# Kernel optimization log

Measured on AMD Instinct MI355X. Metric: run time of the kernel, lower is better.

## Reference

```python
import jax, jax.numpy as jnp
import numpy as np

N_NODES = 100000
N_EDGES = 1600000
IN_CH, HID_CH, OUT_CH = 128, 128, 40


def setup_inputs() -> dict:
    key = jax.random.key(0)
    ks = jax.random.split(key, 7)
    s = 1.0 / np.sqrt(IN_CH)
    s2 = 1.0 / np.sqrt(HID_CH)
    return {
        "x": jax.random.normal(ks[0], (N_NODES, IN_CH), jnp.float32),
        "edge_index": jax.random.randint(ks[1], (2, N_EDGES), 0, N_NODES, jnp.int64),
        "W1l": jax.random.normal(ks[2], (IN_CH, HID_CH), jnp.float32) * s,
        "b1": jnp.zeros((HID_CH,), jnp.float32),
        "W1r": jax.random.normal(ks[3], (IN_CH, HID_CH), jnp.float32) * s,
        "W2l": jax.random.normal(ks[4], (HID_CH, OUT_CH), jnp.float32) * s2,
        "b2": jnp.zeros((OUT_CH,), jnp.float32),
        "W2r": jax.random.normal(ks[5], (HID_CH, OUT_CH), jnp.float32) * s2,
    }


def reference(x, edge_index, W1l, b1, W1r, W2l, b2, W2r):
    src, dst = edge_index[0], edge_index[1]
    # per-target in-degree for mean aggregation (zero-degree nodes -> 0 output)
    deg = jax.ops.segment_sum(jnp.ones((src.shape[0],), x.dtype), dst,
                              num_segments=N_NODES)
    inv_deg = jnp.where(deg > 0, 1.0 / jnp.maximum(deg, 1.0), 0.0)[:, None]

    def sage(h, Wl, b, Wr):
        # gather source features, scatter-sum to targets, normalize -> mean
        agg = jax.ops.segment_sum(h[src], dst, num_segments=N_NODES) * inv_deg
        return agg @ Wl + b + h @ Wr

    h = jax.nn.relu(sage(x, W1l, b1, W1r))
    # F.dropout(p=0.5) defaults to training=True -> active dropout
    keep = jax.random.bernoulli(jax.random.key(42), 0.5, h.shape)
    h = jnp.where(keep, h * 2.0, 0.0)
    out = sage(h, W2l, b2, W2r)
    return jax.nn.log_softmax(out, axis=1)
```

## Files before the change

kernel.cpp:

```cpp
#include <hip/hip_runtime.h>
#include <stdint.h>
#include <stddef.h>

#define N_NODES 100000
#define N_EDGES 1600000
#define IN_CH 128
#define HID_CH 128
#define OUT_CH 40

#define NB 196
#define GCAP 10240
#define TILE_EDGES 2048
#define LCAP 40

#define N_MASK_WORDS 400000
#define N_CVT8 1600000

#define WROW 264
#define WROW2 136

#define QSCALE 21.25f
#define QSTEP  0.047058824f

typedef __attribute__((ext_vector_type(8))) short bf16x8;
typedef __attribute__((ext_vector_type(8))) unsigned short u16x8;
typedef __attribute__((ext_vector_type(4))) float f32x4;

__device__ __forceinline__ ushort f2bf(float f) {
    uint32_t u = __float_as_uint(f);
    uint32_t r = (u + 0x7FFFu + ((u >> 16) & 1u)) >> 16;
    return (ushort)r;
}
__device__ __forceinline__ float bf2f(ushort u) {
    return __uint_as_float(((uint32_t)u) << 16);
}

__device__ __forceinline__ uint32_t rotl32(uint32_t x, int r) {
    return (x << r) | (x >> (32 - r));
}

__device__ __forceinline__ void threefry2x32_k42(uint32_t x0, uint32_t x1,
                                                 uint32_t& o0, uint32_t& o1) {
    const uint32_t ks0 = 0u, ks1 = 42u;
    const uint32_t ks2 = 0u ^ 42u ^ 0x1BD11BDAu;
    x0 += ks0; x1 += ks1;
    x0 += x1; x1 = rotl32(x1, 13); x1 ^= x0;
    x0 += x1; x1 = rotl32(x1, 15); x1 ^= x0;
    x0 += x1; x1 = rotl32(x1, 26); x1 ^= x0;
    x0 += x1; x1 = rotl32(x1,  6); x1 ^= x0;
    x0 += ks1; x1 += ks2 + 1u;
    x0 += x1; x1 = rotl32(x1, 17); x1 ^= x0;
    x0 += x1; x1 = rotl32(x1, 29); x1 ^= x0;
    x0 += x1; x1 = rotl32(x1, 16); x1 ^= x0;
    x0 += x1; x1 = rotl32(x1, 24); x1 ^= x0;
    x0 += ks2; x1 += ks0 + 2u;
    x0 += x1; x1 = rotl32(x1, 13); x1 ^= x0;
    x0 += x1; x1 = rotl32(x1, 15); x1 ^= x0;
    x0 += x1; x1 = rotl32(x1, 26); x1 ^= x0;
    x0 += x1; x1 = rotl32(x1,  6); x1 ^= x0;
    x0 += ks0; x1 += ks1 + 3u;
    x0 += x1; x1 = rotl32(x1, 17); x1 ^= x0;
    x0 += x1; x1 = rotl32(x1, 29); x1 ^= x0;
    x0 += x1; x1 = rotl32(x1, 16); x1 ^= x0;
    x0 += x1; x1 = rotl32(x1, 24); x1 ^= x0;
    x0 += ks1; x1 += ks2 + 4u;
    x0 += x1; x1 = rotl32(x1, 13); x1 ^= x0;
    x0 += x1; x1 = rotl32(x1, 15); x1 ^= x0;
    x0 += x1; x1 = rotl32(x1, 26); x1 ^= x0;
    x0 += x1; x1 = rotl32(x1,  6); x1 ^= x0;
    x0 += ks2; x1 += ks0 + 5u;
    o0 = x0; o1 = x1;
}

__device__ __forceinline__ void load_edge(const void* ei, bool is32, int e,
                                          int& s, int& d) {
    if (is32) {
        const int* p = (const int*)ei;
        s = p[e]; d = p[N_EDGES + e];
    } else {
        const long long* p = (const long long*)ei;
        s = (int)p[e]; d = (int)p[N_EDGES + e];
    }
}

__global__ __launch_bounds__(256) void prep(const int* __restrict__ ei32,
                                            int* __restrict__ flag,
                                            int* __restrict__ gcnt) {
    const int t = threadIdx.x;
    if (blockIdx.x == 0) {
        __shared__ int red[256];
        int local = 0;
        #pragma unroll
        for (int j = 0; j < 64; ++j) {
            int k = (t * 64 + j) * 97;
            local |= ei32[2 * k + 1];
        }
        red[t] = local;
        __syncthreads();
        for (int off = 128; off; off >>= 1) {
            if (t < off) red[t] |= red[t + off];
            __syncthreads();
        }
        if (t == 0) *flag = (red[0] != 0);
    } else {
        for (int i = t; i < NB * 16; i += 256) gcnt[i] = 0;
    }
}

__global__ __launch_bounds__(256) void bucket_edges(
    const void* __restrict__ ei, const int* __restrict__ flag,
    int* __restrict__ gcnt, uint2* __restrict__ gbuf) {
    __shared__ uint2 lbuf[NB][LCAP];
    __shared__ int lcnt[NB];
    const bool is32 = (*flag != 0);
    const int t = threadIdx.x;
    for (int b = t; b < NB; b += 256) lcnt[b] = 0;
    __syncthreads();
    const int base = blockIdx.x * TILE_EDGES;
    #pragma unroll
    for (int j = 0; j < TILE_EDGES / 256; ++j) {
        int e = base + j * 256 + t;
        if (e < N_EDGES) {
            int s, d;
            load_edge(ei, is32, e, s, d);
            int b = d >> 9;
            int pos = atomicAdd(&lcnt[b], 1);
            if (pos < LCAP) {
                lbuf[b][pos] = make_uint2((uint32_t)s, (uint32_t)d);
            } else {
                int gp = atomicAdd(&gcnt[b * 16], 1);
                gbuf[(size_t)b * GCAP + gp] = make_uint2((uint32_t)s, (uint32_t)d);
            }
        }
    }
    __syncthreads();
    if (t < NB) {
        int cnt = lcnt[t];
        if (cnt > LCAP) cnt = LCAP;
        if (cnt > 0) {
            int gp = atomicAdd(&gcnt[t * 16], cnt);
            uint2* dst = gbuf + (size_t)t * GCAP + gp;
            for (int i = 0; i < cnt; ++i) dst[i] = lbuf[t][i];
        }
    }
}

__global__ void bucket_scan(const int* __restrict__ gcnt, int* __restrict__ bbase) {
    __shared__ int s[256];
    int t = threadIdx.x;
    int tot = (t < NB) ? gcnt[t * 16] : 0;
    s[t] = tot;
    __syncthreads();
    for (int off = 1; off < 256; off <<= 1) {
        int a = (t >= off) ? s[t - off] : 0;
        __syncthreads();
        s[t] += a;
        __syncthreads();
    }
    if (t < NB) bbase[t] = s[t] - tot;
}

__global__ __launch_bounds__(256) void build_csr(
    const int* __restrict__ gcnt, const uint2* __restrict__ gbuf,
    const int* __restrict__ bbase, int* __restrict__ csr, int* __restrict__ cursor) {
    __shared__ int hist[512];
    __shared__ int excl[512];
    __shared__ int cur[512];
    __shared__ int psum[256];
    const int b = blockIdx.x;
    const int t = threadIdx.x;
    hist[t] = 0; hist[t + 256] = 0;
    __syncthreads();
    const int base = bbase[b];
    const int cnt = gcnt[b * 16];
    const uint2* src = gbuf + (size_t)b * GCAP;
    for (int i = t; i < cnt; i += 256)
        atomicAdd(&hist[src[i].y & 511], 1);
    __syncthreads();
    int h0 = hist[2 * t], h1 = hist[2 * t + 1];
    psum[t] = h0 + h1;
    __syncthreads();
    int v = psum[t];
    for (int off = 1; off < 256; off <<= 1) {
        int a = (t >= off) ? psum[t - off] : 0;
        __syncthreads();
        psum[t] += a;
        __syncthreads();
    }
    int pex = psum[t] - v;
    excl[2 * t] = pex;
    excl[2 * t + 1] = pex + h0;
    cur[2 * t] = pex;
    cur[2 * t + 1] = pex + h0;
    __syncthreads();
    for (int j = t; j < 512; j += 256) {
        int node = b * 512 + j;
        if (node < N_NODES) cursor[node] = base + excl[j] + hist[j];
    }
    for (int i = t; i < cnt; i += 256) {
        uint2 p = src[i];
        int pos = atomicAdd(&cur[p.y & 511], 1);
        csr[base + pos] = (int)p.x;
    }
}

__device__ __forceinline__ uint32_t q4(float a, float b, float c, float d) {
    int qa = (int)rintf(a * QSCALE + 128.0f);
    int qb = (int)rintf(b * QSCALE + 128.0f);
    int qc = (int)rintf(c * QSCALE + 128.0f);
    int qd = (int)rintf(d * QSCALE + 128.0f);
    qa = min(max(qa, 0), 255);
    qb = min(max(qb, 0), 255);
    qc = min(max(qc, 0), 255);
    qd = min(max(qd, 0), 255);
    return (uint32_t)qa | ((uint32_t)qb << 8) | ((uint32_t)qc << 16) | ((uint32_t)qd << 24);
}

__global__ __launch_bounds__(256) void cvt_and_mask(
    const float* __restrict__ in, ushort* __restrict__ out,
    uint32_t* __restrict__ xu8, uint32_t* __restrict__ mask) {
    const long gid = (long)blockIdx.x * blockDim.x + threadIdx.x;
    const long stride = (long)gridDim.x * blockDim.x;
    for (long i = gid; i < N_CVT8; i += stride) {
        float4 v0 = *reinterpret_cast<const float4*>(in + i * 8);
        float4 v1 = *reinterpret_cast<const float4*>(in + i * 8 + 4);
        u16x8 r;
        r[0] = f2bf(v0.x); r[1] = f2bf(v0.y); r[2] = f2bf(v0.z); r[3] = f2bf(v0.w);
        r[4] = f2bf(v1.x); r[5] = f2bf(v1.y); r[6] = f2bf(v1.z); r[7] = f2bf(v1.w);
        *reinterpret_cast<u16x8*>(out + i * 8) = r;
        uint2 p;
        p.x = q4(v0.x, v0.y, v0.z, v0.w);
        p.y = q4(v1.x, v1.y, v1.z, v1.w);
        *reinterpret_cast<uint2*>(xu8 + i * 2) = p;
    }
    for (long w = gid; w < N_MASK_WORDS; w += stride) {
        uint32_t m = 0;
        #pragma unroll 4
        for (int j = 0; j < 32; ++j) {
            uint32_t o0, o1;
            threefry2x32_k42(0u, (uint32_t)w * 32u + j, o0, o1);
            m |= ((o0 ^ o1) >> 31) << j;
        }
        mask[w] = m;
    }
}

__global__ void cvt_w2(const float* __restrict__ W1l, const float* __restrict__ W1r,
                       const float* __restrict__ W2l, const float* __restrict__ W2r,
                       ushort* __restrict__ Wt1, ushort* __restrict__ Wt2) {
    int blk = blockIdx.x;
    int k = threadIdx.x;
    if (blk < 128) {
        int n = blk;
        float v = (k < 128) ? W1l[(size_t)k * 128 + n] : W1r[(size_t)(k - 128) * 128 + n];
        Wt1[(size_t)n * 256 + k] = f2bf(v);
    } else if (k < 128) {
        int n = blk - 128;
        float v = (n < OUT_CH) ? W2l[(size_t)k * 40 + n]
                               : W2r[(size_t)k * 40 + (n - OUT_CH)];
        Wt2[(size_t)n * 128 + k] = f2bf(v);
    }
}

__global__ __launch_bounds__(256) void aggregate_mean_u8(
    const uint32_t* __restrict__ feat8, const int* __restrict__ csr,
    const int* __restrict__ cursor, ushort* __restrict__ out) {
    int node = blockIdx.x * 4 + (threadIdx.x >> 6);
    if (node >= N_NODES) return;
    const int lane = threadIdx.x & 63;
    const int g = lane >> 4;
    const int c = lane & 15;
    const int beg = (node > 0) ? cursor[node - 1] : 0;
    const int end = cursor[node];
    const int deg = end - beg;

    int myidx = (lane < deg) ? csr[beg + lane] : 0;

    float acc[8];
    #pragma unroll
    for (int j = 0; j < 8; ++j) acc[j] = 0.0f;

    const int nfull = (deg < 64) ? deg : 64;
    const int niter = (nfull + 3) >> 2;
    #pragma unroll 4
    for (int k = 0; k < niter; ++k) {
        int e = g + 4 * k;
        bool valid = (e < nfull);
        int es = valid ? e : 0;
        int s = __shfl(myidx, es, 64);
        float w = valid ? 1.0f : 0.0f;
        uint2 v = *reinterpret_cast<const uint2*>(feat8 + (size_t)s * 32 + c * 2);
        acc[0] += w * (float)(v.x & 0xffu);
        acc[1] += w * (float)((v.x >> 8) & 0xffu);
        acc[2] += w * (float)((v.x >> 16) & 0xffu);
        acc[3] += w * (float)(v.x >> 24);
        acc[4] += w * (float)(v.y & 0xffu);
        acc[5] += w * (float)((v.y >> 8) & 0xffu);
        acc[6] += w * (float)((v.y >> 16) & 0xffu);
        acc[7] += w * (float)(v.y >> 24);
    }
    for (int e = 64 + g; e < deg; e += 4) {
        int s = csr[beg + e];
        uint2 v = *reinterpret_cast<const uint2*>(feat8 + (size_t)s * 32 + c * 2);
        acc[0] += (float)(v.x & 0xffu);
        acc[1] += (float)((v.x >> 8) & 0xffu);
        acc[2] += (float)((v.x >> 16) & 0xffu);
        acc[3] += (float)(v.x >> 24);
        acc[4] += (float)(v.y & 0xffu);
        acc[5] += (float)((v.y >> 8) & 0xffu);
        acc[6] += (float)((v.y >> 16) & 0xffu);
        acc[7] += (float)(v.y >> 24);
    }

    #pragma unroll
    for (int j = 0; j < 8; ++j) {
        acc[j] += __shfl_xor(acc[j], 16, 64);
        acc[j] += __shfl_xor(acc[j], 32, 64);
    }

    if (g == 0) {
        float inv = (deg > 0) ? (1.0f / (float)deg) : 0.0f;
        u16x8 r;
        #pragma unroll
        for (int j = 0; j < 8; ++j) {
            float m = (deg > 0) ? (acc[j] * inv - 128.0f) * QSTEP : 0.0f;
            r[j] = f2bf(m);
        }
        *reinterpret_cast<u16x8*>(out + (size_t)node * 128 + c * 8) = r;
    }
}

__global__ __launch_bounds__(256) void layer1_mfma(
    const ushort* __restrict__ agg, const ushort* __restrict__ xbf,
    const ushort* __restrict__ Wt, const float* __restrict__ b1,
    const uint32_t* __restrict__ dmask, ushort* __restrict__ h) {
    __shared__ ushort wlds[64 * WROW];
    const int tid = threadIdx.x;
    const int lane = tid & 63;
    const int l15 = lane & 15, kg = lane >> 4;
    const int colBase = (blockIdx.x & 1) * 64;
    const int row_base = ((blockIdx.x >> 1) * 4 + (tid >> 6)) * 16;

    #pragma unroll
    for (int i = 0; i < 8; ++i) {
        int idx = tid + i * 256;
        int r = idx >> 5, c = idx & 31;
        u16x8 v = *reinterpret_cast<const u16x8*>(Wt + (size_t)(colBase + r) * 256 + c * 8);
        *reinterpret_cast<u16x8*>(wlds + r * WROW + c * 8) = v;
    }
    __syncthreads();
    if (row_base >= N_NODES) return;

    int r0 = row_base + l15;
    int r0c = (r0 < N_NODES) ? r0 : (N_NODES - 1);

    bf16x8 a[8];
    #pragma unroll
    for (int ks = 0; ks < 4; ++ks) {
        a[ks]     = *reinterpret_cast<const bf16x8*>(agg + (size_t)r0c * 128 + ks * 32 + kg * 8);
        a[ks + 4] = *reinterpret_cast<const bf16x8*>(xbf + (size_t)r0c * 128 + ks * 32 + kg * 8);
    }

    f32x4 acc[4];
    #pragma unroll
    for (int nf = 0; nf < 4; ++nf) acc[nf] = (f32x4){0.f, 0.f, 0.f, 0.f};

    #pragma unroll
    for (int nf = 0; nf < 4; ++nf) {
        const ushort* bp = wlds + (nf * 16 + l15) * WROW + kg * 8;
        #pragma unroll
        for (int ks = 0; ks < 8; ++ks) {
            bf16x8 b = *reinterpret_cast<const bf16x8*>(bp + ks * 32);
            acc[nf] = __builtin_amdgcn_mfma_f32_16x16x32_bf16(a[ks], b, acc[nf], 0, 0, 0);
        }
    }

    #pragma unroll
    for (int r = 0; r < 4; ++r) {
        int row = row_base + kg * 4 + r;
        if (row < N_NODES) {
            uint4 mw = *reinterpret_cast<const uint4*>(dmask + (size_t)row * 4);
            const uint32_t* mwp = reinterpret_cast<const uint32_t*>(&mw);
            #pragma unroll
            for (int nf = 0; nf < 4; ++nf) {
                int col = colBase + nf * 16 + l15;
                float v = acc[nf][r] + b1[col];
                v = fmaxf(v, 0.0f) * 2.0f;
                if ((mwp[col >> 5] >> (col & 31)) & 1u) v = 0.0f;
                h[(size_t)row * 128 + col] = f2bf(v);
            }
        }
    }
}

__global__ __launch_bounds__(256) void layer2_pre(
    const ushort* __restrict__ hbf, const ushort* __restrict__ Wt2,
    ushort* __restrict__ y2z2) {
    __shared__ ushort wlds[80 * WROW2];
    const int tid = threadIdx.x;
    const int lane = tid & 63;
    const int l15 = lane & 15, kg = lane >> 4;
    const int row_base = (blockIdx.x * 4 + (tid >> 6)) * 16;

    #pragma unroll
    for (int i = 0; i < 5; ++i) {
        int idx = tid + i * 256;
        int r = idx >> 4, c = idx & 15;
        u16x8 v = *reinterpret_cast<const u16x8*>(Wt2 + (size_t)r * 128 + c * 8);
        *reinterpret_cast<u16x8*>(wlds + r * WROW2 + c * 8) = v;
    }
    __syncthreads();
    if (row_base >= N_NODES) return;

    int r0 = row_base + l15;
    int r0c = (r0 < N_NODES) ? r0 : (N_NODES - 1);

    bf16x8 a[4];
    #pragma unroll
    for (int ks = 0; ks < 4; ++ks)
        a[ks] = *reinterpret_cast<const bf16x8*>(hbf + (size_t)r0c * 128 + ks * 32 + kg * 8);

    f32x4 acc[5];
    #pragma unroll
    for (int nf = 0; nf < 5; ++nf) acc[nf] = (f32x4){0.f, 0.f, 0.f, 0.f};

    #pragma unroll
    for (int nf = 0; nf < 5; ++nf) {
        const ushort* bp = wlds + (nf * 16 + l15) * WROW2 + kg * 8;
        #pragma unroll
        for (int ks = 0; ks < 4; ++ks) {
            bf16x8 b = *reinterpret_cast<const bf16x8*>(bp + ks * 32);
            acc[nf] = __builtin_amdgcn_mfma_f32_16x16x32_bf16(a[ks], b, acc[nf], 0, 0, 0);
        }
    }

    #pragma unroll
    for (int r = 0; r < 4; ++r) {
        int row = row_base + kg * 4 + r;
        if (row < N_NODES) {
            #pragma unroll
            for (int nf = 0; nf < 5; ++nf) {
                int col = nf * 16 + l15;
                y2z2[(size_t)row * 80 + col] = f2bf(acc[nf][r]);
            }
        }
    }
}

__global__ __launch_bounds__(256) void aggregate_mean_40(
    const ushort* __restrict__ y2, const int* __restrict__ csr,
    const int* __restrict__ cursor, ushort* __restrict__ aggy2) {
    int node = blockIdx.x * 4 + (threadIdx.x >> 6);
    if (node >= N_NODES) return;
    const int lane = threadIdx.x & 63;
    const int g = lane >> 3;
    const int c = lane & 7;
    const int cc = (c < 5) ? c : (c - 5);
    const float cw = (c < 5) ? 1.0f : 0.0f;
    const int beg = (node > 0) ? cursor[node - 1] : 0;
    const int end = cursor[node];
    const int deg = end - beg;

    int myidx = (lane < deg) ? csr[beg + lane] : 0;

    float acc[8];
    #pragma unroll
    for (int j = 0; j < 8; ++j) acc[j] = 0.0f;

    const int nfull = (deg < 64) ? deg : 64;
    const int niter = (nfull + 7) >> 3;
    for (int k = 0; k < niter; ++k) {
        int e = g + 8 * k;
        bool valid = (e < nfull);
        int es = valid ? e : 0;
        int s = __shfl(myidx, es, 64);
        float w = valid ? cw : 0.0f;
        bf16x8 v = *reinterpret_cast<const bf16x8*>(y2 + (size_t)s * 80 + cc * 8);
        #pragma unroll
        for (int j = 0; j < 8; ++j) acc[j] += w * bf2f((ushort)v[j]);
    }
    for (int e = 64 + g; e < deg; e += 8) {
        int s = csr[beg + e];
        bf16x8 v = *reinterpret_cast<const bf16x8*>(y2 + (size_t)s * 80 + cc * 8);
        #pragma unroll
        for (int j = 0; j < 8; ++j) acc[j] += cw * bf2f((ushort)v[j]);
    }

    #pragma unroll
    for (int j = 0; j < 8; ++j) {
        acc[j] += __shfl_xor(acc[j], 8, 64);
        acc[j] += __shfl_xor(acc[j], 16, 64);
        acc[j] += __shfl_xor(acc[j], 32, 64);
    }

    if (lane < 5) {
        float inv = (deg > 0) ? (1.0f / (float)deg) : 0.0f;
        u16x8 r;
        #pragma unroll
        for (int j = 0; j < 8; ++j) r[j] = f2bf(acc[j] * inv);
        *reinterpret_cast<u16x8*>(aggy2 + (size_t)node * 40 + lane * 8) = r;
    }
}

__global__ __launch_bounds__(256) void layer2_post(
    const ushort* __restrict__ aggy2, const ushort* __restrict__ y2z2,
    const float* __restrict__ b2, float* __restrict__ out) {
    int node = blockIdx.x * blockDim.x + threadIdx.x;
    if (node >= N_NODES) return;

    float v[40];
    #pragma unroll
    for (int i = 0; i < 5; ++i) {
        u16x8 av = *reinterpret_cast<const u16x8*>(aggy2 + (size_t)node * 40 + i * 8);
        u16x8 zv = *reinterpret_cast<const u16x8*>(y2z2 + (size_t)node * 80 + 40 + i * 8);
        #pragma unroll
        for (int j = 0; j < 8; ++j)
            v[i * 8 + j] = bf2f((ushort)av[j]) + bf2f((ushort)zv[j]) + b2[i * 8 + j];
    }
    float mx = -1e30f;
    #pragma unroll
    for (int j = 0; j < 40; ++j) mx = fmaxf(mx, v[j]);
    float se = 0.0f;
    #pragma unroll
    for (int j = 0; j < 40; ++j) se += expf(v[j] - mx);
    float lz = mx + logf(se);
    #pragma unroll
    for (int i = 0; i < 10; ++i) {
        float4 r;
        r.x = v[i * 4 + 0] - lz;
        r.y = v[i * 4 + 1] - lz;
        r.z = v[i * 4 + 2] - lz;
        r.w = v[i * 4 + 3] - lz;
        *reinterpret_cast<float4*>(out + (size_t)node * 40 + i * 4) = r;
    }
}

extern "C" void kernel_launch(void* const* d_in, const int* in_sizes, int n_in,
                              void* d_out, int out_size, void* d_ws, size_t ws_size,
                              hipStream_t stream) {
    const float* x   = (const float*)d_in[0];
    const void*  ei  = d_in[1];
    const float* W1l = (const float*)d_in[2];
    const float* b1  = (const float*)d_in[3];
    const float* W1r = (const float*)d_in[4];
    const float* W2l = (const float*)d_in[5];
    const float* b2  = (const float*)d_in[6];
    const float* W2r = (const float*)d_in[7];
    float* out = (float*)d_out;

    char* ws = (char*)d_ws;
    int*      flag   = (int*)ws;
    int*      gcnt   = (int*)(ws + 4096);
    int*      bbase  = (int*)(ws + 106496);
    ushort*   x_bf   = (ushort*)(ws + 131072);
    ushort*   h_bf   = (ushort*)(ws + 131072 + 25600000);
    ushort*   agg_bf = (ushort*)(ws + 131072 + 51200000);
    ushort*   Wt1    = (ushort*)(ws + 131072 + 76800000);
    ushort*   Wt2    = (ushort*)(ws + 131072 + 76865536);
    uint2*    gbuf   = (uint2*)(ws + 77021184);
    uint32_t* dmask  = (uint32_t*)(ws + 93077504);

    uint32_t* x_u8 = (uint32_t*)(ws + 77021184);

    ushort* y2z2  = (ushort*)(ws + 131072 + 51200000);
    ushort* aggy2 = (ushort*)(ws + 131072 + 51200000 + 16000000);

    char* ob = (char*)d_out;
    int* csr    = (int*)ob;
    int* cursor = (int*)(ob + 6400000);

    prep<<<2, 256, 0, stream>>>((const int*)ei, flag, gcnt);
    bucket_edges<<<(N_EDGES + TILE_EDGES - 1) / TILE_EDGES, 256, 0, stream>>>(
        ei, flag, gcnt, gbuf);
    bucket_scan<<<1, 256, 0, stream>>>(gcnt, bbase);
    build_csr<<<NB, 256, 0, stream>>>(gcnt, gbuf, bbase, csr, cursor);

    cvt_and_mask<<<2048, 256, 0, stream>>>(x, x_bf, x_u8, dmask);
    cvt_w2<<<208, 256, 0, stream>>>(W1l, W1r, W2l, W2r, Wt1, Wt2);

    aggregate_mean_u8<<<(N_NODES + 3) / 4, 256, 0, stream>>>(x_u8, csr, cursor, agg_bf);
    layer1_mfma<<<2 * ((N_NODES + 63) / 64), 256, 0, stream>>>(agg_bf, x_bf, Wt1, b1, dmask, h_bf);

    layer2_pre<<<(N_NODES + 63) / 64, 256, 0, stream>>>(h_bf, Wt2, y2z2);
    aggregate_mean_40<<<(N_NODES + 3) / 4, 256, 0, stream>>>(y2z2, csr, cursor, aggy2);
    layer2_post<<<(N_NODES + 255) / 256, 256, 0, stream>>>(aggy2, y2z2, b2, out);
}
```

Before: 262.6 us.

## Fuse layer-2 aggregation with log-softmax and use packed integer accumulation

Layer-2 mean aggregation now computes bias add, residual add and a cross-lane log_softmax in one kernel. This removes the separate post kernel and the aggy2 round trip through memory. The u8 layer-1 aggregation accumulates two bytes per 32-bit word with SWAR adds instead of eight float converts and FMAs. That is safe from overflow for up to 64 edges because 64*255 fits in 16 bits; the tail beyond 64 edges stays in float. CSR and cursor move from the output buffer into workspace, since the fused kernel writes the output while still reading them.

```diff
diff --git a/kernel.cpp b/kernel.cpp
--- a/kernel.cpp
+++ b/kernel.cpp
@@ -276,9 +276,7 @@
 
     int myidx = (lane < deg) ? csr[beg + lane] : 0;
 
-    float acc[8];
-    #pragma unroll
-    for (int j = 0; j < 8; ++j) acc[j] = 0.0f;
+    uint32_t ia0 = 0, ia1 = 0, ia2 = 0, ia3 = 0;
 
     const int nfull = (deg < 64) ? deg : 64;
     const int niter = (nfull + 3) >> 2;
@@ -288,42 +286,56 @@
         bool valid = (e < nfull);
         int es = valid ? e : 0;
         int s = __shfl(myidx, es, 64);
-        float w = valid ? 1.0f : 0.0f;
         uint2 v = *reinterpret_cast<const uint2*>(feat8 + (size_t)s * 32 + c * 2);
-        acc[0] += w * (float)(v.x & 0xffu);
-        acc[1] += w * (float)((v.x >> 8) & 0xffu);
-        acc[2] += w * (float)((v.x >> 16) & 0xffu);
-        acc[3] += w * (float)(v.x >> 24);
-        acc[4] += w * (float)(v.y & 0xffu);
-        acc[5] += w * (float)((v.y >> 8) & 0xffu);
-        acc[6] += w * (float)((v.y >> 16) & 0xffu);
-        acc[7] += w * (float)(v.y >> 24);
-    }
-    for (int e = 64 + g; e < deg; e += 4) {
-        int s = csr[beg + e];
-        uint2 v = *reinterpret_cast<const uint2*>(feat8 + (size_t)s * 32 + c * 2);
-        acc[0] += (float)(v.x & 0xffu);
-        acc[1] += (float)((v.x >> 8) & 0xffu);
-        acc[2] += (float)((v.x >> 16) & 0xffu);
-        acc[3] += (float)(v.x >> 24);
-        acc[4] += (float)(v.y & 0xffu);
-        acc[5] += (float)((v.y >> 8) & 0xffu);
-        acc[6] += (float)((v.y >> 16) & 0xffu);
-        acc[7] += (float)(v.y >> 24);
-    }
-
-    #pragma unroll
-    for (int j = 0; j < 8; ++j) {
-        acc[j] += __shfl_xor(acc[j], 16, 64);
-        acc[j] += __shfl_xor(acc[j], 32, 64);
-    }
+        uint32_t vx = valid ? v.x : 0u;
+        uint32_t vy = valid ? v.y : 0u;
+        ia0 += vx & 0x00FF00FFu;
+        ia1 += (vx >> 8) & 0x00FF00FFu;
+        ia2 += vy & 0x00FF00FFu;
+        ia3 += (vy >> 8) & 0x00FF00FFu;
+    }
+
+    float fs[8] = {0, 0, 0, 0, 0, 0, 0, 0};
+    if (deg > 64) {
+        for (int e = 64 + g; e < deg; e += 4) {
+            int s = csr[beg + e];
+            uint2 v = *reinterpret_cast<const uint2*>(feat8 + (size_t)s * 32 + c * 2);
+            fs[0] += (float)(v.x & 0xffu);
+            fs[1] += (float)((v.x >> 8) & 0xffu);
+            fs[2] += (float)((v.x >> 16) & 0xffu);
+            fs[3] += (float)(v.x >> 24);
+            fs[4] += (float)(v.y & 0xffu);
+            fs[5] += (float)((v.y >> 8) & 0xffu);
+            fs[6] += (float)((v.y >> 16) & 0xffu);
+            fs[7] += (float)(v.y >> 24);
+        }
+        #pragma unroll
+        for (int j = 0; j < 8; ++j) {
+            fs[j] += __shfl_xor(fs[j], 16, 64);
+            fs[j] += __shfl_xor(fs[j], 32, 64);
+        }
+    }
+
+    ia0 += __shfl_xor(ia0, 16, 64); ia0 += __shfl_xor(ia0, 32, 64);
+    ia1 += __shfl_xor(ia1, 16, 64); ia1 += __shfl_xor(ia1, 32, 64);
+    ia2 += __shfl_xor(ia2, 16, 64); ia2 += __shfl_xor(ia2, 32, 64);
+    ia3 += __shfl_xor(ia3, 16, 64); ia3 += __shfl_xor(ia3, 32, 64);
 
     if (g == 0) {
         float inv = (deg > 0) ? (1.0f / (float)deg) : 0.0f;
+        float sum[8];
+        sum[0] = (float)(ia0 & 0xffffu) + fs[0];
+        sum[1] = (float)(ia1 & 0xffffu) + fs[1];
+        sum[2] = (float)(ia0 >> 16)     + fs[2];
+        sum[3] = (float)(ia1 >> 16)     + fs[3];
+        sum[4] = (float)(ia2 & 0xffffu) + fs[4];
+        sum[5] = (float)(ia3 & 0xffffu) + fs[5];
+        sum[6] = (float)(ia2 >> 16)     + fs[6];
+        sum[7] = (float)(ia3 >> 16)     + fs[7];
         u16x8 r;
         #pragma unroll
         for (int j = 0; j < 8; ++j) {
-            float m = (deg > 0) ? (acc[j] * inv - 128.0f) * QSTEP : 0.0f;
+            float m = (deg > 0) ? (sum[j] * inv - 128.0f) * QSTEP : 0.0f;
             r[j] = f2bf(m);
         }
         *reinterpret_cast<u16x8*>(out + (size_t)node * 128 + c * 8) = r;
@@ -447,9 +459,10 @@
     }
 }
 
-__global__ __launch_bounds__(256) void aggregate_mean_40(
+__global__ __launch_bounds__(256) void aggregate_fused_post(
     const ushort* __restrict__ y2, const int* __restrict__ csr,
-    const int* __restrict__ cursor, ushort* __restrict__ aggy2) {
+    const int* __restrict__ cursor, const ushort* __restrict__ y2z2,
+    const float* __restrict__ b2, float* __restrict__ out) {
     int node = blockIdx.x * 4 + (threadIdx.x >> 6);
     if (node >= N_NODES) return;
     const int lane = threadIdx.x & 63;
@@ -493,45 +506,35 @@
         acc[j] += __shfl_xor(acc[j], 32, 64);
     }
 
-    if (lane < 5) {
-        float inv = (deg > 0) ? (1.0f / (float)deg) : 0.0f;
-        u16x8 r;
-        #pragma unroll
-        for (int j = 0; j < 8; ++j) r[j] = f2bf(acc[j] * inv);
-        *reinterpret_cast<u16x8*>(aggy2 + (size_t)node * 40 + lane * 8) = r;
-    }
-}
-
-__global__ __launch_bounds__(256) void layer2_post(
-    const ushort* __restrict__ aggy2, const ushort* __restrict__ y2z2,
-    const float* __restrict__ b2, float* __restrict__ out) {
-    int node = blockIdx.x * blockDim.x + threadIdx.x;
-    if (node >= N_NODES) return;
-
-    float v[40];
-    #pragma unroll
-    for (int i = 0; i < 5; ++i) {
-        u16x8 av = *reinterpret_cast<const u16x8*>(aggy2 + (size_t)node * 40 + i * 8);
-        u16x8 zv = *reinterpret_cast<const u16x8*>(y2z2 + (size_t)node * 80 + 40 + i * 8);
-        #pragma unroll
-        for (int j = 0; j < 8; ++j)
-            v[i * 8 + j] = bf2f((ushort)av[j]) + bf2f((ushort)zv[j]) + b2[i * 8 + j];
-    }
-    float mx = -1e30f;
-    #pragma unroll
-    for (int j = 0; j < 40; ++j) mx = fmaxf(mx, v[j]);
+    const float inv = (deg > 0) ? (1.0f / (float)deg) : 0.0f;
+    u16x8 zv = *reinterpret_cast<const u16x8*>(y2z2 + (size_t)node * 80 + 40 + cc * 8);
+    float v[8];
+    #pragma unroll
+    for (int j = 0; j < 8; ++j)
+        v[j] = acc[j] * inv + bf2f((ushort)zv[j]) + b2[cc * 8 + j];
+
+    float mx = v[0];
+    #pragma unroll
+    for (int j = 1; j < 8; ++j) mx = fmaxf(mx, v[j]);
+    mx = fmaxf(mx, __shfl_xor(mx, 1, 64));
+    mx = fmaxf(mx, __shfl_xor(mx, 2, 64));
+    mx = fmaxf(mx, __shfl_xor(mx, 4, 64));
+
     float se = 0.0f;
     #pragma unroll
-    for (int j = 0; j < 40; ++j) se += expf(v[j] - mx);
+    for (int j = 0; j < 8; ++j) se += expf(v[j] - mx);
+    se *= cw;
+    se += __shfl_xor(se, 1, 64);
+    se += __shfl_xor(se, 2, 64);
+    se += __shfl_xor(se, 4, 64);
     float lz = mx + logf(se);
-    #pragma unroll
-    for (int i = 0; i < 10; ++i) {
-        float4 r;
-        r.x = v[i * 4 + 0] - lz;
-        r.y = v[i * 4 + 1] - lz;
-        r.z = v[i * 4 + 2] - lz;
-        r.w = v[i * 4 + 3] - lz;
-        *reinterpret_cast<float4*>(out + (size_t)node * 40 + i * 4) = r;
+
+    if (g == 0 && c < 5) {
+        float4 r0, r1;
+        r0.x = v[0] - lz; r0.y = v[1] - lz; r0.z = v[2] - lz; r0.w = v[3] - lz;
+        r1.x = v[4] - lz; r1.y = v[5] - lz; r1.z = v[6] - lz; r1.w = v[7] - lz;
+        *reinterpret_cast<float4*>(out + (size_t)node * 40 + c * 8) = r0;
+        *reinterpret_cast<float4*>(out + (size_t)node * 40 + c * 8 + 4) = r1;
     }
 }
 
@@ -559,15 +562,12 @@
     ushort*   Wt2    = (ushort*)(ws + 131072 + 76865536);
     uint2*    gbuf   = (uint2*)(ws + 77021184);
     uint32_t* dmask  = (uint32_t*)(ws + 93077504);
+    int*      csr    = (int*)(ws + 94703616);
+    int*      cursor = (int*)(ws + 101103616);
 
     uint32_t* x_u8 = (uint32_t*)(ws + 77021184);
 
-    ushort* y2z2  = (ushort*)(ws + 131072 + 51200000);
-    ushort* aggy2 = (ushort*)(ws + 131072 + 51200000 + 16000000);
-
-    char* ob = (char*)d_out;
-    int* csr    = (int*)ob;
-    int* cursor = (int*)(ob + 6400000);
+    ushort* y2z2 = (ushort*)(ws + 131072 + 51200000);
 
     prep<<<2, 256, 0, stream>>>((const int*)ei, flag, gcnt);
     bucket_edges<<<(N_EDGES + TILE_EDGES - 1) / TILE_EDGES, 256, 0, stream>>>(
@@ -582,6 +582,6 @@
     layer1_mfma<<<2 * ((N_NODES + 63) / 64), 256, 0, stream>>>(agg_bf, x_bf, Wt1, b1, dmask, h_bf);
 
     layer2_pre<<<(N_NODES + 63) / 64, 256, 0, stream>>>(h_bf, Wt2, y2z2);
-    aggregate_mean_40<<<(N_NODES + 3) / 4, 256, 0, stream>>>(y2z2, csr, cursor, aggy2);
-    layer2_post<<<(N_NODES + 255) / 256, 256, 0, stream>>>(aggy2, y2z2, b2, out);
-}
+    aggregate_fused_post<<<(N_NODES + 3) / 4, 256, 0, stream>>>(y2z2, csr, cursor,
+                                                                y2z2, b2, out);
+}
```

Result: no change. 264.9 us (+0.9%).
